# Optimization experiments

Hardware: AMD Instinct MI355X
Metric: run time of the kernel (lower is better)

## Reference

```python
import jax, jax.numpy as jnp
import numpy as np

NQ = 10          # qubits
NT = 32          # tokens (LCU terms)
DM = 512         # d_model
DEG = 2          # qsvt degree
B = 128          # batch
NPQC = 4 * NQ    # params per PQC application
DIM = 2 ** NQ    # statevector dimension


def ansatz14_spec(q, layers=1):
    spec = []
    for _ in range(layers):
        spec += [('ry', (i,)) for i in range(q)]
        spec += [('crx', (i, (i + 1) % q)) for i in range(q - 1, -1, -1)]
        spec += [('ry', (i,)) for i in range(q)]
        spec += [('crx', (i, (i - 1) % q)) for i in [q - 1] + list(range(q - 1))]
    return spec

SPEC = ansatz14_spec(NQ, 1)


def _gate_ry(theta):
    h = theta * 0.5
    c = jnp.cos(h)
    s = jnp.sin(h)
    m = jnp.stack([jnp.stack([c, -s], -1), jnp.stack([s, c], -1)], -2)
    return m.astype(jnp.complex64)  # (N,2,2)


def _gate_rx(theta):
    h = theta * 0.5
    c = jnp.cos(h).astype(jnp.complex64)
    s = (-1j) * jnp.sin(h).astype(jnp.complex64)
    return jnp.stack([jnp.stack([c, s], -1), jnp.stack([s, c], -1)], -2)


def _apply_1q(state, mats, wire, q):
    # state: (N, 2^q) complex; mats: (N,2,2); wire 0 is most significant bit
    N = state.shape[0]
    a = 2 ** wire
    bdim = 2 ** (q - wire - 1)
    s = state.reshape(N, a, 2, bdim)
    return jnp.einsum('nij,najb->naib', mats, s).reshape(N, 2 ** q)


def _apply_crx(state, theta, c, t, q):
    # controlled-RX: control wire c, target wire t
    N = state.shape[0]
    st = state.reshape((N,) + (2,) * q)
    ax = 1 + c
    s0 = jnp.take(st, 0, axis=ax)   # control = 0 branch: untouched
    s1 = jnp.take(st, 1, axis=ax)   # control = 1 branch: apply RX on target
    tp = t if t < c else t - 1      # target wire position after removing control axis
    s1n = _apply_1q(s1.reshape(N, -1), _gate_rx(theta), tp, q - 1).reshape(s1.shape)
    return jnp.stack([s0, s1n], axis=ax).reshape(N, 2 ** q)


def _apply_pqc(state, params, q):
    # params: (N, NPQC); fixed small gate list -> Python loop is fine
    for k, (fn, w) in enumerate(SPEC):
        th = params[:, k]
        if fn == 'ry':
            state = _apply_1q(state, _gate_ry(th), w[0], q)
        else:
            state = _apply_crx(state, th, w[0], w[1], q)
    return state


def _apply_lcu(states, params, lcu):
    # states: (B, DIM) complex; params: (B, L, NPQC); lcu: (B, L) complex
    Bn, L = lcu.shape
    rep = jnp.repeat(states, L, axis=0)                    # (B*L, DIM)
    st = _apply_pqc(rep, params.reshape(Bn * L, NPQC), NQ)
    return jnp.einsum('bld,bl->bd', st.reshape(Bn, L, DIM), lcu)


def _measure_xyz(state, q):
    # Pauli expectations per wire: order [X_0..X_{q-1}, Y_0.., Z_0..]
    N = state.shape[0]
    xs, ys, zs = [], [], []
    for w in range(q):
        s = state.reshape(N, 2 ** w, 2, -1)
        a0, a1 = s[:, :, 0, :], s[:, :, 1, :]
        cross = jnp.sum(jnp.conj(a0) * a1, axis=(1, 2))
        xs.append(2.0 * jnp.real(cross))
        ys.append(2.0 * jnp.imag(cross))
        zs.append(jnp.sum(jnp.abs(a0) ** 2 - jnp.abs(a1) ** 2, axis=(1, 2)))
    return jnp.stack(xs + ys + zs, axis=1).astype(jnp.float32)  # (B, 3q)


def reference(tokens_emb, W, b, lcu_re, lcu_im, qsvt_coeffs, ff_params):
    Bn, L, D = tokens_emb.shape
    L = min(L, NT)
    pqc_params = tokens_emb[:, :L] @ W.T + b               # (B, L, NPQC)
    lcu = (lcu_re + 1j * lcu_im).astype(jnp.complex64)[:L]
    lcu = lcu / jnp.sum(jnp.abs(lcu))
    lcu_b = jnp.broadcast_to(lcu[None], (Bn, L))
    init = jnp.zeros((Bn, DIM), jnp.complex64).at[:, 0].set(1.0)
    acc = qsvt_coeffs[0].astype(jnp.complex64) * init
    mono = init
    for k in range(1, DEG + 1):
        mono = _apply_lcu(mono, pqc_params, lcu_b)
        acc = acc + qsvt_coeffs[k].astype(jnp.complex64) * mono
    state = acc / jnp.sum(jnp.abs(qsvt_coeffs))
    state = state / jnp.linalg.norm(state, axis=-1, keepdims=True)
    ffp = jnp.broadcast_to(ff_params[None], (Bn, NPQC))
    state = _apply_pqc(state, ffp, NQ)
    return _measure_xyz(state, NQ)


def setup_inputs():
    key = jax.random.key(0)
    ks = jax.random.split(key, 7)
    return {
        'tokens_emb': jax.random.normal(ks[0], (B, NT, DM), jnp.float32),
        'W': jax.random.normal(ks[1], (NPQC, DM), jnp.float32) * 0.05,
        'b': jax.random.normal(ks[2], (NPQC,), jnp.float32),
        'lcu_re': jax.random.normal(ks[3], (NT,), jnp.float32),
        'lcu_im': jax.random.normal(ks[4], (NT,), jnp.float32),
        'qsvt_coeffs': jax.random.normal(ks[5], (DEG + 1,), jnp.float32),
        'ff_params': jax.random.normal(ks[6], (NPQC,), jnp.float32),
    }
```

## Files before the change

kernel.cpp:

```cpp
#include <hip/hip_runtime.h>
#include <hip/hip_bf16.h>


#define NQ   10
#define NT   32
#define DM   512
#define BATCH 128
#define NPQC 40
#define DIM  1024
#define NROWS (BATCH * NT)
#define PSTRIDE (BATCH * DIM)

typedef float v2f __attribute__((ext_vector_type(2)));

#define WAITLDS asm volatile("s_waitcnt lgkmcnt(0)" ::: "memory")

__device__ __forceinline__ v2f Jrot(v2f v) {
  return __builtin_shufflevector(v, -v, 1, 2);
}
__device__ __forceinline__ v2f Jc(v2f v) {
  return __builtin_shufflevector(-v, v, 1, 2);
}


template<int B>
__device__ __forceinline__ void g_ry(v2f (&a)[16], float c, float s) {
  static_assert(B >= 6, "RY targets must be register bits");
  constexpr int m = 1 << (B - 6);
#pragma unroll
  for (int r = 0; r < 16; ++r) {
    if (!(r & m)) {
      int r1 = r | m;
      v2f a0 = a[r], a1 = a[r1];
      a[r]  = c * a0 - s * a1;
      a[r1] = s * a0 + c * a1;
    }
  }
}

template<int BC, int BT>
__device__ __forceinline__ void g_crx(v2f (&a)[16], int lane, float c, float s) {
  static_assert(BT >= 6, "CRX targets must be register bits");
  constexpr int m = 1 << (BT - 6);
  bool lane_ok = (BC >= 6) || ((lane >> BC) & 1);
  float ce = lane_ok ? c : 1.f;
  float se = lane_ok ? s : 0.f;
#pragma unroll
  for (int r = 0; r < 16; ++r) {
    if (!(r & m)) {
      if constexpr (BC >= 6) { if (!((r >> (BC - 6)) & 1)) continue; }
      int r1 = r | m;
      v2f a0 = a[r], a1 = a[r1];
      a[r]  = ce * a0 + se * Jrot(a1);
      a[r1] = ce * a1 + se * Jrot(a0);
    }
  }
}

template<int L0, int L1, int L2, int L3>
__device__ __forceinline__ void remap(v2f (&a)[16], v2f* __restrict__ slab,
                                      int lane) {
  constexpr int LM = (1 << L0) | (1 << L1) | (1 << L2) | (1 << L3);
#pragma unroll
  for (int r = 0; r < 16; ++r) {
    int f = 0;
    if (L0 < 4 && (r & 1)) f |= 1 << L0;
    if (L1 < 4 && (r & 2)) f |= 1 << L1;
    if (L2 < 4 && (r & 4)) f |= 1 << L2;
    if (L3 < 4 && (r & 8)) f |= 1 << L3;
    slab[r * 64 + (lane ^ f)] = a[r];
  }
  WAITLDS;
  int la = lane & ~LM & 63;
  la |= ((lane >> L0) & 1) << 6;
  la |= ((lane >> L1) & 1) << 7;
  la |= ((lane >> L2) & 1) << 8;
  la |= ((lane >> L3) & 1) << 9;
  if (L0 < 4) la |= ((lane >> L0) & 1) << L0;
  if (L1 < 4) la |= ((lane >> L1) & 1) << L1;
  if (L2 < 4) la |= ((lane >> L2) & 1) << L2;
  if (L3 < 4) la |= ((lane >> L3) & 1) << L3;
#pragma unroll
  for (int r = 0; r < 16; ++r) {
    int rc = ((r & 1) ? (1 << L0) : 0) | ((r & 2) ? (1 << L1) : 0)
           | ((r & 4) ? (1 << L2) : 0) | ((r & 8) ? (1 << L3) : 0);
    a[r] = slab[la ^ rc];
  }
}

template<bool SKIP_HEAD>
__device__ __forceinline__ void apply_pqc_phased(v2f (&a)[16],
    const float2* __restrict__ cs, v2f* __restrict__ slab, int lane) {
#define RYt(B, t)      g_ry<B>(a, t.x, t.y);
#define CXt(BC, BT, t) g_crx<BC, BT>(a, lane, t.x, t.y);
  float2 t10 = cs[10], t11 = cs[11], t12 = cs[12];
  if constexpr (!SKIP_HEAD) {
    float2 t0 = cs[0], t1 = cs[1], t2 = cs[2], t3 = cs[3];
    float2 t4 = cs[4], t5 = cs[5], t6 = cs[6], t7 = cs[7];
    float2 t8 = cs[8], t9 = cs[9];
    RYt(9,t0) RYt(8,t1) RYt(7,t2) RYt(6,t3)
    remap<5,4,3,2>(a, slab, lane);
    RYt(6,t4) RYt(7,t5) RYt(8,t6) RYt(9,t7)
    remap<1,0,2,3>(a, slab, lane);
    RYt(6,t8) RYt(7,t9)
  }
  CXt(7,8,t10) CXt(6,7,t11) CXt(3,6,t12)
  float2 t13 = cs[13], t14 = cs[14], t15 = cs[15], t16 = cs[16];
  remap<1,0,2,3>(a, slab, lane);
  CXt(8,9,t13) CXt(7,8,t14) CXt(6,7,t15) CXt(5,6,t16)
  float2 t17 = cs[17], t18 = cs[18], t19 = cs[19];
  float2 t20 = cs[20], t21 = cs[21], t22 = cs[22], t23 = cs[23];
  remap<2,3,4,5>(a, slab, lane);
  CXt(8,9,t17) CXt(7,8,t18) CXt(6,7,t19)
  RYt(6,t20) RYt(7,t21) RYt(8,t22) RYt(9,t23)
  float2 t24 = cs[24], t25 = cs[25], t26 = cs[26], t27 = cs[27];
  remap<2,3,4,5>(a, slab, lane);
  RYt(6,t24) RYt(7,t25) RYt(8,t26) RYt(9,t27)
  float2 t28 = cs[28], t29 = cs[29];
  float2 t30 = cs[30], t31 = cs[31], t32 = cs[32], t33 = cs[33];
  remap<1,0,2,3>(a, slab, lane);
  RYt(6,t28) RYt(7,t29)
  CXt(7,6,t30) CXt(8,7,t31) CXt(9,8,t32) CXt(4,9,t33)
  float2 t34 = cs[34], t35 = cs[35], t36 = cs[36], t37 = cs[37];
  remap<4,5,1,0>(a, slab, lane);
  CXt(7,6,t34) CXt(8,7,t35) CXt(9,8,t36) CXt(2,9,t37)
  float2 t38 = cs[38], t39 = cs[39];
  remap<2,3,4,5>(a, slab, lane);
  CXt(7,6,t38) CXt(8,7,t39)
#undef RYt
#undef CXt
}

__device__ __forceinline__ int p8_lane_canon(int lane) {
  return (((lane >> 1) & 1) << 9) | ((lane & 1) << 8) | (((lane >> 2) & 1) << 7)
       | (((lane >> 3) & 1) << 6) | (((lane >> 4) & 1) << 5) | (((lane >> 5) & 1) << 4);
}

__device__ __forceinline__ void stagger(int key) {
  int s = key & 3;
  if (s & 1) __builtin_amdgcn_s_sleep(1);
  if (s & 2) __builtin_amdgcn_s_sleep(2);
}

__global__ __launch_bounds__(256) void params_kernel(
    const float* __restrict__ emb, const float* __restrict__ W,
    const float* __restrict__ bias,
    const float* __restrict__ lcu_re, const float* __restrict__ lcu_im,
    const float* __restrict__ ffp,
    float2* __restrict__ cs, float2* __restrict__ ffcs, float2* __restrict__ lcu) {
  int blk = blockIdx.x;
  int tid = threadIdx.x;
  if (blk == 256) {
    if (tid < NPQC) {
      float h = 0.5f * ffp[tid];
      ffcs[tid] = make_float2(cosf(h), sinf(h));
    }
    if (tid == 64) {
      float ssum = 0.f;
      for (int i = 0; i < NT; ++i) {
        float re = lcu_re[i], im = lcu_im[i];
        ssum += sqrtf(re * re + im * im);
      }
      float inv = 1.f / ssum;
      for (int i = 0; i < NT; ++i)
        lcu[i] = make_float2(lcu_re[i] * inv, lcu_im[i] * inv);
    }
    return;
  }

  __shared__ float Asl[16 * 516];
  int row0 = blk * 16;

  const float4* eg = (const float4*)(emb + (size_t)row0 * DM);
#pragma unroll
  for (int i = 0; i < 8; ++i) {
    int e = tid + i * 256;
    int r = e >> 7, k4 = e & 127;
    float4 v = eg[e];
    *(float4*)&Asl[r * 516 + k4 * 4] = v;
  }
  __syncthreads();

  int kq = tid >> 6;
  int lane = tid & 63;
  int rg = lane >> 3;
  int cg = lane & 7;

  const float* Ar0 = &Asl[(2 * rg) * 516 + kq * 128];
  const float* Ar1 = Ar0 + 516;
  const float* Bg  = W + (size_t)(5 * cg) * DM + kq * 128;

  float acc[2][5] = {};
#pragma unroll 4
  for (int k = 0; k < 128; k += 4) {
    float4 a0 = *(const float4*)(Ar0 + k);
    float4 a1 = *(const float4*)(Ar1 + k);
#pragma unroll
    for (int j = 0; j < 5; ++j) {
      float4 b = *(const float4*)(Bg + j * DM + k);
      acc[0][j] += a0.x * b.x + a0.y * b.y + a0.z * b.z + a0.w * b.w;
      acc[1][j] += a1.x * b.x + a1.y * b.y + a1.z * b.z + a1.w * b.w;
    }
  }

  __syncthreads();
  float* red = Asl;
#pragma unroll
  for (int i = 0; i < 2; ++i)
#pragma unroll
    for (int j = 0; j < 5; ++j)
      red[kq * 644 + (2 * rg + i) * 40 + 5 * cg + j] = acc[i][j];
  __syncthreads();

  for (int o = tid; o < 640; o += 256) {
    float v = bias[o % 40] + red[o] + red[644 + o] + red[1288 + o] + red[1932 + o];
    float h = 0.5f * v;
    cs[(size_t)blk * 640 + o] = make_float2(cosf(h), sinf(h));
  }
}

template<bool FIRST>
__global__ __launch_bounds__(256) void pqc_step(
    const float2* __restrict__ cs, const float2* __restrict__ lcu,
    const v2f* __restrict__ src, v2f* __restrict__ dst) {
  __shared__ v2f slabs[4][1024];
  int lane = threadIdx.x & 63;
  int wvu = __builtin_amdgcn_readfirstlane(threadIdx.x >> 6);
  int blk = blockIdx.x;
  stagger(blk + wvu);
  int b = blk >> 3, qq = blk & 7;
  int l = qq * 4 + wvu;
  const float2* csrow = cs + (size_t)(b * NT + l) * NPQC;
  v2f* slab = slabs[wvu];

  v2f a[16];
  if constexpr (FIRST) {
    float2 f5 = csrow[5], f4 = csrow[4], f6 = csrow[6], f7 = csrow[7];
    float2 f2 = csrow[2], f3 = csrow[3];
    float2 f8 = csrow[8], f9 = csrow[9], f0 = csrow[0], f1 = csrow[1];
    float lp = ((lane & 1) ? f5.y : f5.x);
    lp *= ((lane & 2) ? f4.y : f4.x);
    lp *= ((lane & 4) ? f6.y : f6.x);
    lp *= ((lane & 8) ? f7.y : f7.x);
    lp *= ((lane & 16) ? f2.y : f2.x);
    lp *= ((lane & 32) ? f3.y : f3.x);
#pragma unroll
    for (int r = 0; r < 16; ++r) {
      float rp = ((r & 1) ? f8.y : f8.x) * ((r & 2) ? f9.y : f9.x)
               * ((r & 4) ? f0.y : f0.x) * ((r & 8) ? f1.y : f1.x);
      a[r].x = lp * rp;
      a[r].y = 0.f;
    }
  } else {
    const v2f* s = src + (size_t)b * DIM;
#pragma unroll
    for (int r = 0; r < 16; ++r) a[r] = s[r * 64 + lane];
  }

  apply_pqc_phased<FIRST>(a, csrow, slab, lane);

  float2 w = lcu[l];
  int pl = p8_lane_canon(lane);
  pl ^= (pl >> 5);
#pragma unroll
  for (int r = 0; r < 16; ++r) {
    int rc = ((r & 1) << 3) | ((r & 2) << 1) | ((r & 4) >> 1) | ((r & 8) >> 3);
    slab[pl ^ rc] = w.x * a[r] + w.y * Jc(a[r]);
  }
  __syncthreads();

  v2f* dst_b = dst + (size_t)(qq * BATCH + b) * DIM;
#pragma unroll
  for (int i = 0; i < 4; ++i) {
    int n = threadIdx.x + i * 256;
    int ph = n ^ (n >> 5);
    v2f sum = slabs[0][ph] + slabs[1][ph] + slabs[2][ph] + slabs[3][ph];
    dst_b[n] = sum;
  }
}


__global__ __launch_bounds__(256) void reduce_slices(v2f* __restrict__ buf) {
  int n = blockIdx.x * 256 + threadIdx.x;
  v2f acc = buf[n];
#pragma unroll
  for (int q = 1; q < 8; ++q) acc += buf[n + q * PSTRIDE];
  buf[n] = acc;
}

__global__ __launch_bounds__(256) void final_reduce(
    const v2f* __restrict__ red1, v2f* __restrict__ part2,
    const float* __restrict__ qsvt) {
  __shared__ float rbuf[4];
  int b = blockIdx.x, tid = threadIdx.x;
  int lane = tid & 63, wv = tid >> 6;
  float q0 = qsvt[0], q1 = qsvt[1], q2 = qsvt[2];
  const v2f* r1 = red1 + (size_t)b * DIM;
  v2f* p2 = part2 + (size_t)b * DIM;

  v2f vals[4];
  float nn = 0.f;
#pragma unroll
  for (int i = 0; i < 4; ++i) {
    int n = tid + i * 256;
    v2f m2 = p2[n];
#pragma unroll
    for (int q = 1; q < 8; ++q) m2 += p2[n + q * PSTRIDE];
    v2f v = q1 * r1[n] + q2 * m2;
    if (n == 0) v.x += q0;
    vals[i] = v;
    nn += v.x * v.x + v.y * v.y;
  }
#pragma unroll
  for (int o = 1; o < 64; o <<= 1) nn += __shfl_xor(nn, o);
  if (lane == 0) rbuf[wv] = nn;
  __syncthreads();
  float inv = 1.f / sqrtf(rbuf[0] + rbuf[1] + rbuf[2] + rbuf[3]);
#pragma unroll
  for (int i = 0; i < 4; ++i) p2[tid + i * 256] = vals[i] * inv;
}

__global__ __launch_bounds__(64) void final_pqc(
    const v2f* __restrict__ state, const float2* __restrict__ ffcs,
    float* __restrict__ out) {
  __shared__ v2f slab[1024];
  int lane = threadIdx.x;
  int b = blockIdx.x;

  v2f a[16];
  const v2f* s = state + (size_t)b * DIM;
#pragma unroll
  for (int r = 0; r < 16; ++r) a[r] = s[r * 64 + lane];

  apply_pqc_phased<false>(a, ffcs, slab, lane);

  constexpr int BPOS[10] = {1, 0, 2, 3, 4, 5, 6, 7, 8, 9};
  float prt[30];
#pragma unroll
  for (int w = 0; w < NQ; ++w) {
    const int p = BPOS[w];
    float xr = 0.f, xi = 0.f, zz = 0.f;
    if (p >= 6) {
      const int m = 1 << (p - 6);
#pragma unroll
      for (int r = 0; r < 16; ++r) {
        float mag = a[r].x * a[r].x + a[r].y * a[r].y;
        zz += (r & m) ? -mag : mag;
        if (!(r & m)) {
          int r1 = r | m;
          xr += a[r].x * a[r1].x + a[r].y * a[r1].y;
          xi += a[r].x * a[r1].y - a[r].y * a[r1].x;
        }
      }
    } else {
      const int lm = 1 << p;
      bool lo = !(lane & lm);
#pragma unroll
      for (int r = 0; r < 16; ++r) {
        float mag = a[r].x * a[r].x + a[r].y * a[r].y;
        zz += lo ? mag : -mag;
        float pr = __shfl_xor(a[r].x, lm);
        float pi = __shfl_xor(a[r].y, lm);
        if (lo) {
          xr += a[r].x * pr + a[r].y * pi;
          xi += a[r].x * pi - a[r].y * pr;
        }
      }
    }
    prt[w]      = xr;
    prt[10 + w] = xi;
    prt[20 + w] = zz;
  }

  float* tb = (float*)slab;
#pragma unroll
  for (int v = 0; v < 30; ++v) tb[v * 65 + lane] = prt[v];
  WAITLDS;
  if (lane < 30) {
    float s2 = 0.f;
#pragma unroll
    for (int k = 0; k < 64; ++k) s2 += tb[lane * 65 + k];
    float sc = (lane < 20) ? 2.f : 1.f;
    out[b * 30 + lane] = sc * s2;
  }
}


extern "C" void kernel_launch(void* const* d_in, const int* in_sizes, int n_in,
                              void* d_out, int out_size, void* d_ws, size_t ws_size,
                              hipStream_t stream) {
  const float* emb    = (const float*)d_in[0];
  const float* W      = (const float*)d_in[1];
  const float* bias   = (const float*)d_in[2];
  const float* lcu_re = (const float*)d_in[3];
  const float* lcu_im = (const float*)d_in[4];
  const float* qsvt   = (const float*)d_in[5];
  const float* ffp    = (const float*)d_in[6];
  float* out = (float*)d_out;

  char* ws = (char*)d_ws;
  float2* cs    = (float2*)ws;
  float2* ffcs  = (float2*)(ws + 1310720);
  float2* lcu   = (float2*)(ws + 1311040);
  v2f*    part1 = (v2f*)(ws + 1311744);
  v2f*    part2 = (v2f*)(ws + 1311744 + 8388608);

  params_kernel<<<257, 256, 0, stream>>>(emb, W, bias, lcu_re, lcu_im, ffp,
                                         cs, ffcs, lcu);
  pqc_step<true><<<1024, 256, 0, stream>>>(cs, lcu, nullptr, part1);
  reduce_slices<<<512, 256, 0, stream>>>(part1);
  pqc_step<false><<<1024, 256, 0, stream>>>(cs, lcu, part1, part2);
  final_reduce<<<BATCH, 256, 0, stream>>>(part1, part2, qsvt);
  final_pqc<<<BATCH, 64, 0, stream>>>(part2, ffcs, out);
}
```

Before: 154.3 us.

## Rewrite final PQC as gate-by-gate LDS-resident statevector with swizzled indexing

The final feed-forward PQC kernel no longer keeps the state in registers with a phased layout. It now stores the 1024-amplitude state in shared memory under an XOR swizzle and applies the 40 gates one at a time in a rolled loop, each gate reading and writing amplitude pairs through LDS. The measurement loop also reads pairs from LDS instead of using register shuffles. The goal is lower register pressure and code size in exchange for many more LDS round trips. This kernel handles only one of several stages, so the effect on total time is likely small.

```diff
diff --git a/kernel.cpp b/kernel.cpp
--- a/kernel.cpp
+++ b/kernel.cpp
@@ -320,66 +320,92 @@
   for (int i = 0; i < 4; ++i) p2[tid + i * 256] = vals[i] * inv;
 }
 
-__global__ __launch_bounds__(64) void final_pqc(
+__global__ __launch_bounds__(64, 1) void final_pqc(
     const v2f* __restrict__ state, const float2* __restrict__ ffcs,
     float* __restrict__ out) {
-  __shared__ v2f slab[1024];
+  __shared__ v2f st[1024];
+  __shared__ float2 ang[40];
+  __shared__ float tb[30 * 65];
   int lane = threadIdx.x;
   int b = blockIdx.x;
 
-  v2f a[16];
   const v2f* s = state + (size_t)b * DIM;
 #pragma unroll
-  for (int r = 0; r < 16; ++r) a[r] = s[r * 64 + lane];
-
-  apply_pqc_phased<false>(a, ffcs, slab, lane);
-
-  constexpr int BPOS[10] = {1, 0, 2, 3, 4, 5, 6, 7, 8, 9};
-  float prt[30];
-#pragma unroll
+  for (int r = 0; r < 16; ++r) {
+    int n = r * 64 + lane;
+    st[n ^ (n >> 5)] = s[n];
+  }
+  if (lane < NPQC) ang[lane] = ffcs[lane];
+  WAITLDS;
+
+#pragma unroll 1
+  for (int k = 0; k < NPQC; ++k) {
+    int isCrx, c, t;
+    if (k < 10)      { isCrx = 0; t = k;      c = 0; }
+    else if (k < 20) { int i = 19 - k; isCrx = 1; c = i; t = (i == 9) ? 0 : i + 1; }
+    else if (k < 30) { isCrx = 0; t = k - 20; c = 0; }
+    else             { int i = (k == 30) ? 9 : k - 31; isCrx = 1; c = i; t = (i == 0) ? 9 : i - 1; }
+    int m  = 1 << (9 - t);
+    int cb = 9 - c;
+    float2 th = ang[k];
+    float cg = th.x, sg = th.y;
+
+    v2f a0[8], a1[8];
+    int j0[8], j1[8], en[8];
+#pragma unroll
+    for (int p = 0; p < 8; ++p) {
+      int q  = p * 64 + lane;
+      int i0 = ((q & ~(m - 1)) << 1) | (q & (m - 1));
+      int i1 = i0 | m;
+      j0[p] = i0 ^ (i0 >> 5);
+      j1[p] = i1 ^ (i1 >> 5);
+      en[p] = (i0 >> cb) & 1;
+      a0[p] = st[j0[p]];
+      a1[p] = st[j1[p]];
+    }
+    WAITLDS;
+#pragma unroll
+    for (int p = 0; p < 8; ++p) {
+      v2f n0, n1;
+      if (!isCrx) {
+        n0 = cg * a0[p] - sg * a1[p];
+        n1 = sg * a0[p] + cg * a1[p];
+      } else {
+        float ce = en[p] ? cg : 1.f;
+        float se = en[p] ? sg : 0.f;
+        n0 = ce * a0[p] + se * Jrot(a1[p]);
+        n1 = ce * a1[p] + se * Jrot(a0[p]);
+      }
+      st[j0[p]] = n0;
+      st[j1[p]] = n1;
+    }
+    WAITLDS;
+  }
+
+#pragma unroll 1
   for (int w = 0; w < NQ; ++w) {
-    const int p = BPOS[w];
+    int m = 1 << (9 - w);
     float xr = 0.f, xi = 0.f, zz = 0.f;
-    if (p >= 6) {
-      const int m = 1 << (p - 6);
-#pragma unroll
-      for (int r = 0; r < 16; ++r) {
-        float mag = a[r].x * a[r].x + a[r].y * a[r].y;
-        zz += (r & m) ? -mag : mag;
-        if (!(r & m)) {
-          int r1 = r | m;
-          xr += a[r].x * a[r1].x + a[r].y * a[r1].y;
-          xi += a[r].x * a[r1].y - a[r].y * a[r1].x;
-        }
-      }
-    } else {
-      const int lm = 1 << p;
-      bool lo = !(lane & lm);
-#pragma unroll
-      for (int r = 0; r < 16; ++r) {
-        float mag = a[r].x * a[r].x + a[r].y * a[r].y;
-        zz += lo ? mag : -mag;
-        float pr = __shfl_xor(a[r].x, lm);
-        float pi = __shfl_xor(a[r].y, lm);
-        if (lo) {
-          xr += a[r].x * pr + a[r].y * pi;
-          xi += a[r].x * pi - a[r].y * pr;
-        }
-      }
-    }
-    prt[w]      = xr;
-    prt[10 + w] = xi;
-    prt[20 + w] = zz;
-  }
-
-  float* tb = (float*)slab;
-#pragma unroll
-  for (int v = 0; v < 30; ++v) tb[v * 65 + lane] = prt[v];
+#pragma unroll
+    for (int p = 0; p < 8; ++p) {
+      int q  = p * 64 + lane;
+      int i0 = ((q & ~(m - 1)) << 1) | (q & (m - 1));
+      int i1 = i0 | m;
+      v2f a0 = st[i0 ^ (i0 >> 5)];
+      v2f a1 = st[i1 ^ (i1 >> 5)];
+      xr += a0.x * a1.x + a0.y * a1.y;
+      xi += a0.x * a1.y - a0.y * a1.x;
+      zz += a0.x * a0.x + a0.y * a0.y - a1.x * a1.x - a1.y * a1.y;
+    }
+    tb[w * 65 + lane]        = xr;
+    tb[(10 + w) * 65 + lane] = xi;
+    tb[(20 + w) * 65 + lane] = zz;
+  }
   WAITLDS;
   if (lane < 30) {
     float s2 = 0.f;
 #pragma unroll
-    for (int k = 0; k < 64; ++k) s2 += tb[lane * 65 + k];
+    for (int k2 = 0; k2 < 64; ++k2) s2 += tb[lane * 65 + k2];
     float sc = (lane < 20) ? 2.f : 1.f;
     out[b * 30 + lane] = sc * s2;
   }
```

Result: slower. 166.7 us (+8.0%).
